# Optimization experiments

Hardware: AMD Instinct MI355X
Metric: run time of the kernel (lower is better)

The kernel has to match this reference:

```python
import jax, jax.numpy as jnp
import numpy as np
import math

H = 16          # num heads
D = 64          # size_per_head
HID = H * D     # 1024
ROT = 32        # rotary_hsize <= D//2


def setup_inputs() -> dict:
    key = jax.random.key(0)
    ks = jax.random.split(key, 10)
    B, S = 2, 2048
    x = jax.random.normal(ks[0], (B, S, HID), dtype=jnp.float32)
    sinusoids = jax.random.normal(ks[1], (B, 2, S, ROT), dtype=jnp.float32)
    attention_bias = jnp.zeros((B, 1, S, S), dtype=jnp.float32)
    scale = 1.0 / math.sqrt(HID)
    Wq = jax.random.normal(ks[2], (HID, HID), dtype=jnp.float32) * scale
    bq = jnp.zeros((HID,), dtype=jnp.float32)
    Wk = jax.random.normal(ks[3], (HID, HID), dtype=jnp.float32) * scale
    bk = jnp.zeros((HID,), dtype=jnp.float32)
    Wv = jax.random.normal(ks[4], (HID, HID), dtype=jnp.float32) * scale
    bv = jnp.zeros((HID,), dtype=jnp.float32)
    Wo = jax.random.normal(ks[5], (HID, HID), dtype=jnp.float32) * scale
    return {"x": x, "sinusoids": sinusoids, "attention_bias": attention_bias,
            "Wq": Wq, "bq": bq, "Wk": Wk, "bk": bk, "Wv": Wv, "bv": bv, "Wo": Wo}


def _apply_rotary(qk, sin, cos):
    # qk: [B,S,H,D]; sin/cos: [B,S,1,ROT]
    r = qk[..., :ROT]
    # stack([-even, odd], -1).reshape -> interleaved (-x0, x1, -x2, x3, ...)
    rt = jnp.stack([-r[..., ::2], r[..., 1::2]], axis=-1).reshape(r.shape)
    return jnp.concatenate([r * cos + rt * sin, qk[..., ROT:]], axis=-1)


def reference(x, sinusoids, attention_bias, Wq, bq, Wk, bk, Wv, bv, Wo):
    B, S, _ = x.shape
    q = (x @ Wq + bq).reshape(B, S, H, D)
    k = (x @ Wk + bk).reshape(B, S, H, D)
    v = (x @ Wv + bv).reshape(B, S, H, D)
    sin = sinusoids[..., 0, :, None, :]  # [B,S,1,ROT]
    cos = sinusoids[..., 1, :, None, :]
    q = _apply_rotary(q, sin, cos)
    k = _apply_rotary(k, sin, cos)
    q = q / math.sqrt(D)
    scores = jnp.einsum('bqhd,bkhd->bhqk', q, k) + attention_bias
    probs = jax.nn.softmax(scores, axis=-1)
    out = jnp.einsum('bhqk,bkhd->bqhd', probs, v).reshape(B, S, HID)
    return out @ Wo
```

## Files before the change

### kernel.cpp

```cpp
#include <hip/hip_runtime.h>
#include <hip/hip_bf16.h>

#define H_   16
#define D_   64
#define HID  1024
#define S_   2048
#define B_   2
#define M_   (B_*S_)
#define ROT  32
#define LOG2E 1.44269504088896341f
#define QSCALE (0.125f * LOG2E)

typedef __bf16 bf16x8 __attribute__((ext_vector_type(8)));
typedef float  f32x4  __attribute__((ext_vector_type(4)));

#define XB_OFF   0u
#define WQT_OFF  (8u<<20)
#define WKT_OFF  (10u<<20)
#define WVT_OFF  (12u<<20)
#define WOT_OFF  (14u<<20)
#define F_OFF    (16u<<20)
#define QH_OFF   ((16u<<20) + (1u<<19))
#define KH_OFF   (QH_OFF + (8u<<20))
#define VT_OFF   (KH_OFF + (8u<<20))
#define AB_OFF   (VT_OFF + (8u<<20))

__device__ __forceinline__ float fexp2(float x) {
#if __has_builtin(__builtin_amdgcn_exp2f)
  return __builtin_amdgcn_exp2f(x);
#else
  return __expf(x * 0.69314718055994531f);
#endif
}

__device__ __forceinline__ unsigned pk2(float a, float b) {
  union { unsigned u; __bf16 h[2]; } w;
  w.h[0] = (__bf16)a; w.h[1] = (__bf16)b;
  return w.u;
}

__global__ __launch_bounds__(256) void prep_kernel(const float* __restrict__ x,
                                                   const float* __restrict__ sinu,
                                                   const float* __restrict__ abias,
                                                   const float* __restrict__ W0, const float* __restrict__ W1,
                                                   const float* __restrict__ W2, const float* __restrict__ W3,
                                                   __hip_bfloat16* __restrict__ xb,
                                                   float* __restrict__ F,
                                                   __hip_bfloat16* __restrict__ T0, __hip_bfloat16* __restrict__ T1,
                                                   __hip_bfloat16* __restrict__ T2, __hip_bfloat16* __restrict__ T3,
                                                   int* __restrict__ flag) {
  __shared__ float tile[32][33];
  int idx = blockIdx.x;
  int tid = threadIdx.x;
  if (idx < 4096) {
    int i = (idx * 256 + tid) * 4;
    float4 v = *(const float4*)(x + i);
    union { __hip_bfloat16 h[4]; uint2 u; } o;
    o.h[0] = __float2bfloat16(v.x);
    o.h[1] = __float2bfloat16(v.y);
    o.h[2] = __float2bfloat16(v.z);
    o.h[3] = __float2bfloat16(v.w);
    *(uint2*)(xb + i) = o.u;
  } else if (idx < 4608) {
    int i = (idx - 4096) * 256 + tid;
    int d  = i & (ROT-1);
    int bs = i >> 5;
    int s  = bs & (S_-1);
    int b  = bs >> 11;
    float sn = sinu[(((size_t)b*2 + 0)*S_ + s)*ROT + d];
    float cs = sinu[(((size_t)b*2 + 1)*S_ + s)*ROT + d];
    F[i] = cs + ((d & 1) ? sn : -sn);
  } else if (idx < 8704) {
    int widx = idx - 4608;
    int z    = widx >> 10;
    int rem  = widx & 1023;
    const float* W = (z==0) ? W0 : (z==1) ? W1 : (z==2) ? W2 : W3;
    __hip_bfloat16* T = (z==0) ? T0 : (z==1) ? T1 : (z==2) ? T2 : T3;
    int bx = (rem & 31) * 32;
    int by = (rem >> 5) * 32;
    int tx = tid & 31, ty = tid >> 5;
    #pragma unroll
    for (int i = 0; i < 4; i++)
      tile[ty + i*8][tx] = W[(size_t)(by + ty + i*8)*HID + bx + tx];
    __syncthreads();
    #pragma unroll
    for (int i = 0; i < 4; i++)
      T[(size_t)(bx + ty + i*8)*HID + by + tx] = __float2bfloat16(tile[tx][ty + i*8]);
  } else {
    size_t i = ((size_t)(idx - 8704) * 256 + tid) * 16;
    const uint4* p = (const uint4*)(abias + i);
    unsigned acc = 0;
    #pragma unroll
    for (int j = 0; j < 4; j++) {
      uint4 u = p[j];
      acc |= u.x | u.y | u.z | u.w;
    }
    if (acc) *flag = 1;
  }
}

__global__ __launch_bounds__(256) void qkv_kernel(const __hip_bfloat16* __restrict__ A,
                                                  const __hip_bfloat16* __restrict__ Bt,
                                                  const float* __restrict__ bq,
                                                  const float* __restrict__ bk,
                                                  const float* __restrict__ bv,
                                                  const float* __restrict__ F,
                                                  __hip_bfloat16* __restrict__ Qh,
                                                  __hip_bfloat16* __restrict__ Kh,
                                                  __hip_bfloat16* __restrict__ Vt) {
  __shared__ __align__(16) __bf16 Asm[2][128*32];
  __shared__ __align__(16) __bf16 Bsm[2][128*32];
  int tid  = threadIdx.x;
  int lane = tid & 63;
  int wv   = tid >> 6;
  int lr   = lane & 15;
  int qd   = lane >> 4;
  int row0 = blockIdx.y * 128;
  int col0 = blockIdx.x * 128;
  int wrow = (wv >> 1) * 64;
  int wcol = (wv & 1) * 64;

  int cg = ((tid & 3) ^ ((tid >> 2) & 3)) * 8;
  const __bf16* Ag = (const __bf16*)A  + (size_t)(row0 + (tid >> 2)) * HID + cg;
  const __bf16* Bg = (const __bf16*)Bt + (size_t)(col0 + (tid >> 2)) * HID + cg;

  f32x4 acc[4][4] = {};

  auto stage = [&](int buf, int k0) {
    __builtin_amdgcn_global_load_lds(Ag + k0,                  &Asm[buf][wv*512],        16, 0, 0);
    __builtin_amdgcn_global_load_lds(Ag + (size_t)64*HID + k0, &Asm[buf][2048 + wv*512], 16, 0, 0);
    __builtin_amdgcn_global_load_lds(Bg + k0,                  &Bsm[buf][wv*512],        16, 0, 0);
    __builtin_amdgcn_global_load_lds(Bg + (size_t)64*HID + k0, &Bsm[buf][2048 + wv*512], 16, 0, 0);
  };

  stage(0, 0);
  int buf = 0;
  for (int k0 = 0; k0 < HID; k0 += 32, buf ^= 1) {
    __syncthreads();
    if (k0 + 32 < HID) stage(buf ^ 1, k0 + 32);
    const __bf16* As = &Asm[buf][0];
    const __bf16* Bs = &Bsm[buf][0];
    bf16x8 a[4], b[4];
    #pragma unroll
    for (int i = 0; i < 4; i++) {
      int row = wrow + i*16 + lr;
      a[i] = *(const bf16x8*)(As + row*32 + ((qd ^ (row & 3)) * 8));
    }
    #pragma unroll
    for (int t = 0; t < 4; t++) {
      int row = wcol + t*16 + lr;
      b[t] = *(const bf16x8*)(Bs + row*32 + ((qd ^ (row & 3)) * 8));
    }
    #pragma unroll
    for (int i = 0; i < 4; i++)
      #pragma unroll
      for (int t = 0; t < 4; t++)
        acc[i][t] = __builtin_amdgcn_mfma_f32_16x16x32_bf16(a[i], b[t], acc[i][t], 0, 0, 0);
  }

  int proj = col0 >> 10;
  int nb   = (col0 & 1023) + wcol;
  const float* bias = (proj == 0) ? bq : ((proj == 1) ? bk : bv);
  #pragma unroll
  for (int i = 0; i < 4; i++) {
    #pragma unroll
    for (int t = 0; t < 4; t++) {
      int nl = nb + t*16 + lr;
      int h  = nl >> 6, d = nl & 63;
      if (proj == 2) {
        int m0 = row0 + wrow + i*16 + qd*4;
        int b2 = m0 >> 11, s0 = m0 & (S_-1);
        union { uint2 u; __bf16 hh[4]; } w;
        #pragma unroll
        for (int r = 0; r < 4; r++)
          w.hh[r] = (__bf16)(acc[i][t][r] + bias[nl]);
        int pos = (s0 & ~31) | ((s0 & 12) << 1) | ((s0 >> 2) & 4);
        *(uint2*)((__bf16*)Vt + ((size_t)(b2*H_ + h)*D_ + d)*S_ + pos) = w.u;
      } else {
        __hip_bfloat16* dst = (proj == 0) ? Qh : Kh;
        #pragma unroll
        for (int r = 0; r < 4; r++) {
          int m = row0 + wrow + i*16 + qd*4 + r;
          int b2 = m >> 11, s = m & (S_-1);
          float v = acc[i][t][r] + bias[nl];
          if (d < ROT) v *= F[(size_t)(b2*S_ + s)*ROT + d];
          if (proj == 0) v *= QSCALE;
          dst[((size_t)(b2*H_ + h)*S_ + s)*D_ + d] = __float2bfloat16(v);
        }
      }
    }
  }
}

__global__ __launch_bounds__(256) void gemm_o64(const __hip_bfloat16* __restrict__ A,
                                                const __hip_bfloat16* __restrict__ Bt,
                                                float* __restrict__ outf) {
  __shared__ __align__(16) __bf16 Asm[2][128*32];
  __shared__ __align__(16) __bf16 Bsm[2][64*32];
  int tid  = threadIdx.x;
  int lane = tid & 63;
  int wv   = tid >> 6;
  int lr   = lane & 15;
  int qd   = lane >> 4;
  int row0 = blockIdx.y * 128;
  int col0 = blockIdx.x * 64;
  int cg = ((tid & 3) ^ ((tid >> 2) & 3)) * 8;
  const __bf16* Ag = (const __bf16*)A  + (size_t)(row0 + (tid >> 2)) * HID + cg;
  const __bf16* Bg = (const __bf16*)Bt + (size_t)(col0 + (tid >> 2)) * HID + cg;

  f32x4 acc[2][4] = {};
  auto stage = [&](int buf, int k0) {
    __builtin_amdgcn_global_load_lds(Ag + k0,                  &Asm[buf][wv*512],        16, 0, 0);
    __builtin_amdgcn_global_load_lds(Ag + (size_t)64*HID + k0, &Asm[buf][2048 + wv*512], 16, 0, 0);
    __builtin_amdgcn_global_load_lds(Bg + k0,                  &Bsm[buf][wv*512],        16, 0, 0);
  };
  stage(0, 0);
  int buf = 0;
  for (int k0 = 0; k0 < HID; k0 += 32, buf ^= 1) {
    __syncthreads();
    if (k0 + 32 < HID) stage(buf ^ 1, k0 + 32);
    const __bf16* As = &Asm[buf][0];
    const __bf16* Bs = &Bsm[buf][0];
    bf16x8 a[2], b[4];
    #pragma unroll
    for (int i = 0; i < 2; i++) {
      int row = wv*32 + i*16 + lr;
      a[i] = *(const bf16x8*)(As + row*32 + ((qd ^ (row & 3)) * 8));
    }
    #pragma unroll
    for (int t = 0; t < 4; t++) {
      int row = t*16 + lr;
      b[t] = *(const bf16x8*)(Bs + row*32 + ((qd ^ (row & 3)) * 8));
    }
    #pragma unroll
    for (int i = 0; i < 2; i++)
      #pragma unroll
      for (int t = 0; t < 4; t++)
        acc[i][t] = __builtin_amdgcn_mfma_f32_16x16x32_bf16(a[i], b[t], acc[i][t], 0, 0, 0);
  }
  #pragma unroll
  for (int i = 0; i < 2; i++)
    #pragma unroll
    for (int t = 0; t < 4; t++)
      #pragma unroll
      for (int r = 0; r < 4; r++) {
        int m = row0 + wv*32 + i*16 + qd*4 + r;
        int n = col0 + t*16 + lr;
        outf[(size_t)m*HID + n] = acc[i][t][r];
      }
}

__global__ __launch_bounds__(256) void flash_kernel(const __hip_bfloat16* __restrict__ Qh,
                                                    const __hip_bfloat16* __restrict__ Kh,
                                                    const __hip_bfloat16* __restrict__ Vt,
                                                    const float* __restrict__ abias,
                                                    const int* __restrict__ flag,
                                                    __hip_bfloat16* __restrict__ Ab) {
  __shared__ __align__(16) __bf16 Ksm[2][64*64];
  __shared__ __align__(16) __bf16 Vsm[2][64*64];
  int tid  = threadIdx.x;
  int lane = tid & 63;
  int wv   = tid >> 6;
  int lr   = lane & 15;
  int qd   = lane >> 4;
  int idx  = blockIdx.x;
  int xcd  = idx & 7;
  int slot = idx >> 3;
  int bh   = xcd * 4 + (slot >> 4);
  int qblk = slot & 15;
  int b  = bh >> 4;
  int h  = bh & 15;
  int q0 = qblk * 128 + wv * 32;

  const __bf16* Kbase = (const __bf16*)Kh + (size_t)bh*S_*D_;
  const __bf16* Vbase = (const __bf16*)Vt + (size_t)bh*D_*S_;

  const __bf16* Qp = (const __bf16*)Qh + ((size_t)bh*S_ + q0 + lr)*D_ + qd*8;
  bf16x8 qa00 = *(const bf16x8*)(Qp);
  bf16x8 qa01 = *(const bf16x8*)(Qp + 32);
  bf16x8 qa10 = *(const bf16x8*)(Qp + 16*D_);
  bf16x8 qa11 = *(const bf16x8*)(Qp + 16*D_ + 32);

  int hasbias = *flag;
  const float* bp0 = abias + (size_t)b*S_*S_ + (size_t)(q0 + lr)*S_;
  const float* bp1 = bp0 + (size_t)16*S_;

  int rowb = tid >> 3;
  int cg8  = ((tid & 7) ^ (rowb & 7)) * 8;

  auto stageKV = [&](int bf, int kt2) {
    __builtin_amdgcn_global_load_lds(Kbase + (size_t)(kt2 + rowb)*D_ + cg8,      &Ksm[bf][wv*512],        16, 0, 0);
    __builtin_amdgcn_global_load_lds(Kbase + (size_t)(kt2 + 32 + rowb)*D_ + cg8, &Ksm[bf][2048 + wv*512], 16, 0, 0);
    __builtin_amdgcn_global_load_lds(Vbase + (size_t)rowb*S_ + kt2 + cg8,        &Vsm[bf][wv*512],        16, 0, 0);
    __builtin_amdgcn_global_load_lds(Vbase + (size_t)(32 + rowb)*S_ + kt2 + cg8, &Vsm[bf][2048 + wv*512], 16, 0, 0);
  };

  f32x4 oacc0[4] = {}, oacc1[4] = {};
  float lsum0 = 0.f, lsum1 = 0.f;
  int sw = lr & 7;

  union Pu { bf16x8 v; unsigned u[4]; };
  Pu pb00 = {}, pb01 = {}, pb10 = {}, pb11 = {};
  bf16x8 vp0[4], vp1[4];

  stageKV(0, 0);
  int buf = 0;
  for (int kt = 0; kt < S_; kt += 64, buf ^= 1) {
    __syncthreads();
    if (kt + 64 < S_) stageKV(buf ^ 1, kt + 64);

    bf16x8 kf0[4], kf1[4];
    #pragma unroll
    for (int c = 0; c < 4; c++) {
      const __bf16* Kr = &Ksm[buf][(c*16 + lr)*64];
      kf0[c] = *(const bf16x8*)(Kr + ((qd       ^ sw) * 8));
      kf1[c] = *(const bf16x8*)(Kr + (((4 + qd) ^ sw) * 8));
    }

    if (kt > 0) {
      __builtin_amdgcn_s_setprio(1);
      #pragma unroll
      for (int t = 0; t < 4; t++) {
        oacc0[t] = __builtin_amdgcn_mfma_f32_16x16x32_bf16(vp0[t], pb00.v, oacc0[t], 0, 0, 0);
        oacc0[t] = __builtin_amdgcn_mfma_f32_16x16x32_bf16(vp1[t], pb01.v, oacc0[t], 0, 0, 0);
        oacc1[t] = __builtin_amdgcn_mfma_f32_16x16x32_bf16(vp0[t], pb10.v, oacc1[t], 0, 0, 0);
        oacc1[t] = __builtin_amdgcn_mfma_f32_16x16x32_bf16(vp1[t], pb11.v, oacc1[t], 0, 0, 0);
      }
      __builtin_amdgcn_s_setprio(0);
    }

    f32x4 s0[4], s1[4];
    __builtin_amdgcn_s_setprio(1);
    #pragma unroll
    for (int c = 0; c < 4; c++) {
      f32x4 z = {};
      z     = __builtin_amdgcn_mfma_f32_16x16x32_bf16(kf0[c], qa00, z, 0, 0, 0);
      s0[c] = __builtin_amdgcn_mfma_f32_16x16x32_bf16(kf1[c], qa01, z, 0, 0, 0);
      f32x4 z2 = {};
      z2    = __builtin_amdgcn_mfma_f32_16x16x32_bf16(kf0[c], qa10, z2, 0, 0, 0);
      s1[c] = __builtin_amdgcn_mfma_f32_16x16x32_bf16(kf1[c], qa11, z2, 0, 0, 0);
    }
    __builtin_amdgcn_s_setprio(0);

    if (hasbias) {
      #pragma unroll
      for (int c = 0; c < 4; c++) {
        float4 b0 = *(const float4*)(bp0 + kt + c*16 + qd*4);
        float4 b1 = *(const float4*)(bp1 + kt + c*16 + qd*4);
        s0[c][0] += b0.x*LOG2E; s0[c][1] += b0.y*LOG2E; s0[c][2] += b0.z*LOG2E; s0[c][3] += b0.w*LOG2E;
        s1[c][0] += b1.x*LOG2E; s1[c][1] += b1.y*LOG2E; s1[c][2] += b1.z*LOG2E; s1[c][3] += b1.w*LOG2E;
      }
    }

    #pragma unroll
    for (int c = 0; c < 2; c++) {
      float p0 = fexp2(s0[c][0]), p1 = fexp2(s0[c][1]), p2 = fexp2(s0[c][2]), p3 = fexp2(s0[c][3]);
      lsum0 += (p0 + p1) + (p2 + p3);
      pb00.u[2*c]   = pk2(p0, p1);
      pb00.u[2*c+1] = pk2(p2, p3);
      float r0 = fexp2(s1[c][0]), r1 = fexp2(s1[c][1]), r2 = fexp2(s1[c][2]), r3 = fexp2(s1[c][3]);
      lsum1 += (r0 + r1) + (r2 + r3);
      pb10.u[2*c]   = pk2(r0, r1);
      pb10.u[2*c+1] = pk2(r2, r3);
    }
    #pragma unroll
    for (int c = 2; c < 4; c++) {
      float p0 = fexp2(s0[c][0]), p1 = fexp2(s0[c][1]), p2 = fexp2(s0[c][2]), p3 = fexp2(s0[c][3]);
      lsum0 += (p0 + p1) + (p2 + p3);
      pb01.u[2*(c-2)]   = pk2(p0, p1);
      pb01.u[2*(c-2)+1] = pk2(p2, p3);
      float r0 = fexp2(s1[c][0]), r1 = fexp2(s1[c][1]), r2 = fexp2(s1[c][2]), r3 = fexp2(s1[c][3]);
      lsum1 += (r0 + r1) + (r2 + r3);
      pb11.u[2*(c-2)]   = pk2(r0, r1);
      pb11.u[2*(c-2)+1] = pk2(r2, r3);
    }

    #pragma unroll
    for (int t = 0; t < 4; t++) {
      const __bf16* Vr = &Vsm[buf][(t*16 + lr)*64];
      vp0[t] = *(const bf16x8*)(Vr + ((qd       ^ sw) * 8));
      vp1[t] = *(const bf16x8*)(Vr + (((4 + qd) ^ sw) * 8));
    }
  }

  __builtin_amdgcn_s_setprio(1);
  #pragma unroll
  for (int t = 0; t < 4; t++) {
    oacc0[t] = __builtin_amdgcn_mfma_f32_16x16x32_bf16(vp0[t], pb00.v, oacc0[t], 0, 0, 0);
    oacc0[t] = __builtin_amdgcn_mfma_f32_16x16x32_bf16(vp1[t], pb01.v, oacc0[t], 0, 0, 0);
    oacc1[t] = __builtin_amdgcn_mfma_f32_16x16x32_bf16(vp0[t], pb10.v, oacc1[t], 0, 0, 0);
    oacc1[t] = __builtin_amdgcn_mfma_f32_16x16x32_bf16(vp1[t], pb11.v, oacc1[t], 0, 0, 0);
  }
  __builtin_amdgcn_s_setprio(0);

  lsum0 += __shfl_xor(lsum0, 16); lsum0 += __shfl_xor(lsum0, 32);
  lsum1 += __shfl_xor(lsum1, 16); lsum1 += __shfl_xor(lsum1, 32);
  float inv0 = 1.0f / lsum0;
  float inv1 = 1.0f / lsum1;
  size_t ro0 = ((size_t)(b*S_ + q0 + lr))*HID + h*D_;
  size_t ro1 = ((size_t)(b*S_ + q0 + 16 + lr))*HID + h*D_;
  #pragma unroll
  for (int t = 0; t < 4; t++) {
    union { uint2 u; __bf16 hh[4]; } w0, w1;
    #pragma unroll
    for (int r = 0; r < 4; r++) {
      w0.hh[r] = (__bf16)(oacc0[t][r]*inv0);
      w1.hh[r] = (__bf16)(oacc1[t][r]*inv1);
    }
    *(uint2*)((__bf16*)Ab + ro0 + t*16 + qd*4) = w0.u;
    *(uint2*)((__bf16*)Ab + ro1 + t*16 + qd*4) = w1.u;
  }
}

extern "C" void kernel_launch(void* const* d_in, const int* in_sizes, int n_in,
                              void* d_out, int out_size, void* d_ws, size_t ws_size,
                              hipStream_t stream) {
  (void)in_sizes; (void)n_in; (void)out_size; (void)ws_size;
  const float* x     = (const float*)d_in[0];
  const float* sinu  = (const float*)d_in[1];
  const float* abias = (const float*)d_in[2];
  const float* Wq    = (const float*)d_in[3];
  const float* bq    = (const float*)d_in[4];
  const float* Wk    = (const float*)d_in[5];
  const float* bk    = (const float*)d_in[6];
  const float* Wv    = (const float*)d_in[7];
  const float* bv    = (const float*)d_in[8];
  const float* Wo    = (const float*)d_in[9];

  char* ws = (char*)d_ws;
  __hip_bfloat16* Xb  = (__hip_bfloat16*)(ws + XB_OFF);
  __hip_bfloat16* Wqt = (__hip_bfloat16*)(ws + WQT_OFF);
  __hip_bfloat16* Wkt = (__hip_bfloat16*)(ws + WKT_OFF);
  __hip_bfloat16* Wvt = (__hip_bfloat16*)(ws + WVT_OFF);
  __hip_bfloat16* Wot = (__hip_bfloat16*)(ws + WOT_OFF);
  float*          F   = (float*)(ws + F_OFF);
  __hip_bfloat16* Qh  = (__hip_bfloat16*)(ws + QH_OFF);
  __hip_bfloat16* Kh  = (__hip_bfloat16*)(ws + KH_OFF);
  __hip_bfloat16* Vt  = (__hip_bfloat16*)(ws + VT_OFF);
  __hip_bfloat16* Ab  = (__hip_bfloat16*)(ws + AB_OFF);
  int* flag = (int*)d_out;

  hipMemsetAsync(flag, 0, 4, stream);
  prep_kernel<<<10752, 256, 0, stream>>>(x, sinu, abias, Wq, Wk, Wv, Wo,
                                         Xb, F, Wqt, Wkt, Wvt, Wot, flag);

  qkv_kernel<<<dim3(3*HID/128, M_/128), 256, 0, stream>>>(
      Xb, Wqt, bq, bk, bv, F, Qh, Kh, Vt);

  flash_kernel<<<dim3(512), 256, 0, stream>>>(Qh, Kh, Vt, abias, flag, Ab);

  gemm_o64<<<dim3(HID/64, M_/128), 256, 0, stream>>>(Ab, Wot, (float*)d_out);
}
```

Before: 220.1 us.

## Halve flash-attention query tile per wave and double grid for occupancy

Each wave in the attention kernel now handles 16 query rows instead of 32, so a block covers 64 queries and the grid doubles to 1024 blocks, with launch bounds requesting 4 blocks per CU. The aim is more parallelism and fewer registers per thread, giving better latency hiding with 512 blocks on a 256-CU part. In exchange, every K/V tile staged into LDS is reused by half as many queries, which doubles K/V global traffic and the LDS fragment reads per unit of MFMA work.

```diff
diff --git a/kernel.cpp b/kernel.cpp
--- a/kernel.cpp
+++ b/kernel.cpp
@@ -250,7 +250,7 @@
       }
 }
 
-__global__ __launch_bounds__(256) void flash_kernel(const __hip_bfloat16* __restrict__ Qh,
+__global__ __launch_bounds__(256, 4) void flash_kernel(const __hip_bfloat16* __restrict__ Qh,
                                                     const __hip_bfloat16* __restrict__ Kh,
                                                     const __hip_bfloat16* __restrict__ Vt,
                                                     const float* __restrict__ abias,
@@ -266,11 +266,11 @@
   int idx  = blockIdx.x;
   int xcd  = idx & 7;
   int slot = idx >> 3;
-  int bh   = xcd * 4 + (slot >> 4);
-  int qblk = slot & 15;
+  int bh   = xcd * 4 + (slot >> 5);
+  int qblk = slot & 31;
   int b  = bh >> 4;
   int h  = bh & 15;
-  int q0 = qblk * 128 + wv * 32;
+  int q0 = qblk * 64 + wv * 16;
 
   const __bf16* Kbase = (const __bf16*)Kh + (size_t)bh*S_*D_;
   const __bf16* Vbase = (const __bf16*)Vt + (size_t)bh*D_*S_;
@@ -278,12 +278,9 @@
   const __bf16* Qp = (const __bf16*)Qh + ((size_t)bh*S_ + q0 + lr)*D_ + qd*8;
   bf16x8 qa00 = *(const bf16x8*)(Qp);
   bf16x8 qa01 = *(const bf16x8*)(Qp + 32);
-  bf16x8 qa10 = *(const bf16x8*)(Qp + 16*D_);
-  bf16x8 qa11 = *(const bf16x8*)(Qp + 16*D_ + 32);
 
   int hasbias = *flag;
   const float* bp0 = abias + (size_t)b*S_*S_ + (size_t)(q0 + lr)*S_;
-  const float* bp1 = bp0 + (size_t)16*S_;
 
   int rowb = tid >> 3;
   int cg8  = ((tid & 7) ^ (rowb & 7)) * 8;
@@ -295,12 +292,12 @@
     __builtin_amdgcn_global_load_lds(Vbase + (size_t)(32 + rowb)*S_ + kt2 + cg8, &Vsm[bf][2048 + wv*512], 16, 0, 0);
   };
 
-  f32x4 oacc0[4] = {}, oacc1[4] = {};
-  float lsum0 = 0.f, lsum1 = 0.f;
+  f32x4 oacc0[4] = {};
+  float lsum0 = 0.f;
   int sw = lr & 7;
 
   union Pu { bf16x8 v; unsigned u[4]; };
-  Pu pb00 = {}, pb01 = {}, pb10 = {}, pb11 = {};
+  Pu pb00 = {}, pb01 = {};
   bf16x8 vp0[4], vp1[4];
 
   stageKV(0, 0);
@@ -323,22 +320,17 @@
       for (int t = 0; t < 4; t++) {
         oacc0[t] = __builtin_amdgcn_mfma_f32_16x16x32_bf16(vp0[t], pb00.v, oacc0[t], 0, 0, 0);
         oacc0[t] = __builtin_amdgcn_mfma_f32_16x16x32_bf16(vp1[t], pb01.v, oacc0[t], 0, 0, 0);
-        oacc1[t] = __builtin_amdgcn_mfma_f32_16x16x32_bf16(vp0[t], pb10.v, oacc1[t], 0, 0, 0);
-        oacc1[t] = __builtin_amdgcn_mfma_f32_16x16x32_bf16(vp1[t], pb11.v, oacc1[t], 0, 0, 0);
       }
       __builtin_amdgcn_s_setprio(0);
     }
 
-    f32x4 s0[4], s1[4];
+    f32x4 s0[4];
     __builtin_amdgcn_s_setprio(1);
     #pragma unroll
     for (int c = 0; c < 4; c++) {
       f32x4 z = {};
       z     = __builtin_amdgcn_mfma_f32_16x16x32_bf16(kf0[c], qa00, z, 0, 0, 0);
       s0[c] = __builtin_amdgcn_mfma_f32_16x16x32_bf16(kf1[c], qa01, z, 0, 0, 0);
-      f32x4 z2 = {};
-      z2    = __builtin_amdgcn_mfma_f32_16x16x32_bf16(kf0[c], qa10, z2, 0, 0, 0);
-      s1[c] = __builtin_amdgcn_mfma_f32_16x16x32_bf16(kf1[c], qa11, z2, 0, 0, 0);
     }
     __builtin_amdgcn_s_setprio(0);
 
@@ -346,9 +338,7 @@
       #pragma unroll
       for (int c = 0; c < 4; c++) {
         float4 b0 = *(const float4*)(bp0 + kt + c*16 + qd*4);
-        float4 b1 = *(const float4*)(bp1 + kt + c*16 + qd*4);
         s0[c][0] += b0.x*LOG2E; s0[c][1] += b0.y*LOG2E; s0[c][2] += b0.z*LOG2E; s0[c][3] += b0.w*LOG2E;
-        s1[c][0] += b1.x*LOG2E; s1[c][1] += b1.y*LOG2E; s1[c][2] += b1.z*LOG2E; s1[c][3] += b1.w*LOG2E;
       }
     }
 
@@ -358,10 +348,6 @@
       lsum0 += (p0 + p1) + (p2 + p3);
       pb00.u[2*c]   = pk2(p0, p1);
       pb00.u[2*c+1] = pk2(p2, p3);
-      float r0 = fexp2(s1[c][0]), r1 = fexp2(s1[c][1]), r2 = fexp2(s1[c][2]), r3 = fexp2(s1[c][3]);
-      lsum1 += (r0 + r1) + (r2 + r3);
-      pb10.u[2*c]   = pk2(r0, r1);
-      pb10.u[2*c+1] = pk2(r2, r3);
     }
     #pragma unroll
     for (int c = 2; c < 4; c++) {
@@ -369,10 +355,6 @@
       lsum0 += (p0 + p1) + (p2 + p3);
       pb01.u[2*(c-2)]   = pk2(p0, p1);
       pb01.u[2*(c-2)+1] = pk2(p2, p3);
-      float r0 = fexp2(s1[c][0]), r1 = fexp2(s1[c][1]), r2 = fexp2(s1[c][2]), r3 = fexp2(s1[c][3]);
-      lsum1 += (r0 + r1) + (r2 + r3);
-      pb11.u[2*(c-2)]   = pk2(r0, r1);
-      pb11.u[2*(c-2)+1] = pk2(r2, r3);
     }
 
     #pragma unroll
@@ -388,27 +370,19 @@
   for (int t = 0; t < 4; t++) {
     oacc0[t] = __builtin_amdgcn_mfma_f32_16x16x32_bf16(vp0[t], pb00.v, oacc0[t], 0, 0, 0);
     oacc0[t] = __builtin_amdgcn_mfma_f32_16x16x32_bf16(vp1[t], pb01.v, oacc0[t], 0, 0, 0);
-    oacc1[t] = __builtin_amdgcn_mfma_f32_16x16x32_bf16(vp0[t], pb10.v, oacc1[t], 0, 0, 0);
-    oacc1[t] = __builtin_amdgcn_mfma_f32_16x16x32_bf16(vp1[t], pb11.v, oacc1[t], 0, 0, 0);
   }
   __builtin_amdgcn_s_setprio(0);
 
   lsum0 += __shfl_xor(lsum0, 16); lsum0 += __shfl_xor(lsum0, 32);
-  lsum1 += __shfl_xor(lsum1, 16); lsum1 += __shfl_xor(lsum1, 32);
   float inv0 = 1.0f / lsum0;
-  float inv1 = 1.0f / lsum1;
   size_t ro0 = ((size_t)(b*S_ + q0 + lr))*HID + h*D_;
-  size_t ro1 = ((size_t)(b*S_ + q0 + 16 + lr))*HID + h*D_;
   #pragma unroll
   for (int t = 0; t < 4; t++) {
-    union { uint2 u; __bf16 hh[4]; } w0, w1;
-    #pragma unroll
-    for (int r = 0; r < 4; r++) {
+    union { uint2 u; __bf16 hh[4]; } w0;
+    #pragma unroll
+    for (int r = 0; r < 4; r++)
       w0.hh[r] = (__bf16)(oacc0[t][r]*inv0);
-      w1.hh[r] = (__bf16)(oacc1[t][r]*inv1);
-    }
     *(uint2*)((__bf16*)Ab + ro0 + t*16 + qd*4) = w0.u;
-    *(uint2*)((__bf16*)Ab + ro1 + t*16 + qd*4) = w1.u;
   }
 }
 
@@ -447,7 +421,7 @@
   qkv_kernel<<<dim3(3*HID/128, M_/128), 256, 0, stream>>>(
       Xb, Wqt, bq, bk, bv, F, Qh, Kh, Vt);
 
-  flash_kernel<<<dim3(512), 256, 0, stream>>>(Qh, Kh, Vt, abias, flag, Ab);
+  flash_kernel<<<dim3(1024), 256, 0, stream>>>(Qh, Kh, Vt, abias, flag, Ab);
 
   gemm_o64<<<dim3(HID/64, M_/128), 256, 0, stream>>>(Ab, Wot, (float*)d_out);
 }
```

New measurement: 226.6 us. 1.03x slower.

## Split flash attention KV range across two wave groups per block and merge

Applied to the files above, without the earlier changes.

Doubles the flash kernel block to 512 threads. Each half of the block processes half of the key/value sequence for the same 128 query rows, using its own double-buffered LDS. At the end, the second half writes its partial output accumulators and row sums into LDS, and the first half merges them and normalizes. This raises wave count per block to improve latency hiding and CU utilisation on a 512-block grid. The cost is double the LDS, an extra merge through LDS, and two more barriers. The merge skips max rescaling because the softmax here uses no running max.

```diff
diff --git a/kernel.cpp b/kernel.cpp
--- a/kernel.cpp
+++ b/kernel.cpp
@@ -250,17 +250,19 @@
       }
 }
 
-__global__ __launch_bounds__(256) void flash_kernel(const __hip_bfloat16* __restrict__ Qh,
+__global__ __launch_bounds__(512, 4) void flash_kernel(const __hip_bfloat16* __restrict__ Qh,
                                                     const __hip_bfloat16* __restrict__ Kh,
                                                     const __hip_bfloat16* __restrict__ Vt,
                                                     const float* __restrict__ abias,
                                                     const int* __restrict__ flag,
                                                     __hip_bfloat16* __restrict__ Ab) {
-  __shared__ __align__(16) __bf16 Ksm[2][64*64];
-  __shared__ __align__(16) __bf16 Vsm[2][64*64];
+  __shared__ __align__(16) __bf16 Ksm[2][2][64*64];
+  __shared__ __align__(16) __bf16 Vsm[2][2][64*64];
   int tid  = threadIdx.x;
   int lane = tid & 63;
   int wv   = tid >> 6;
+  int wvh  = wv & 3;
+  int kh   = wv >> 2;
   int lr   = lane & 15;
   int qd   = lane >> 4;
   int idx  = blockIdx.x;
@@ -270,7 +272,8 @@
   int qblk = slot & 15;
   int b  = bh >> 4;
   int h  = bh & 15;
-  int q0 = qblk * 128 + wv * 32;
+  int q0 = qblk * 128 + wvh * 32;
+  int kt0 = kh * (S_/2);
 
   const __bf16* Kbase = (const __bf16*)Kh + (size_t)bh*S_*D_;
   const __bf16* Vbase = (const __bf16*)Vt + (size_t)bh*D_*S_;
@@ -285,14 +288,15 @@
   const float* bp0 = abias + (size_t)b*S_*S_ + (size_t)(q0 + lr)*S_;
   const float* bp1 = bp0 + (size_t)16*S_;
 
-  int rowb = tid >> 3;
-  int cg8  = ((tid & 7) ^ (rowb & 7)) * 8;
+  int tidh = tid & 255;
+  int rowb = tidh >> 3;
+  int cg8  = ((tidh & 7) ^ (rowb & 7)) * 8;
 
   auto stageKV = [&](int bf, int kt2) {
-    __builtin_amdgcn_global_load_lds(Kbase + (size_t)(kt2 + rowb)*D_ + cg8,      &Ksm[bf][wv*512],        16, 0, 0);
-    __builtin_amdgcn_global_load_lds(Kbase + (size_t)(kt2 + 32 + rowb)*D_ + cg8, &Ksm[bf][2048 + wv*512], 16, 0, 0);
-    __builtin_amdgcn_global_load_lds(Vbase + (size_t)rowb*S_ + kt2 + cg8,        &Vsm[bf][wv*512],        16, 0, 0);
-    __builtin_amdgcn_global_load_lds(Vbase + (size_t)(32 + rowb)*S_ + kt2 + cg8, &Vsm[bf][2048 + wv*512], 16, 0, 0);
+    __builtin_amdgcn_global_load_lds(Kbase + (size_t)(kt2 + rowb)*D_ + cg8,      &Ksm[kh][bf][wvh*512],        16, 0, 0);
+    __builtin_amdgcn_global_load_lds(Kbase + (size_t)(kt2 + 32 + rowb)*D_ + cg8, &Ksm[kh][bf][2048 + wvh*512], 16, 0, 0);
+    __builtin_amdgcn_global_load_lds(Vbase + (size_t)rowb*S_ + kt2 + cg8,        &Vsm[kh][bf][wvh*512],        16, 0, 0);
+    __builtin_amdgcn_global_load_lds(Vbase + (size_t)(32 + rowb)*S_ + kt2 + cg8, &Vsm[kh][bf][2048 + wvh*512], 16, 0, 0);
   };
 
   f32x4 oacc0[4] = {}, oacc1[4] = {};
@@ -303,21 +307,21 @@
   Pu pb00 = {}, pb01 = {}, pb10 = {}, pb11 = {};
   bf16x8 vp0[4], vp1[4];
 
-  stageKV(0, 0);
+  stageKV(0, kt0);
   int buf = 0;
-  for (int kt = 0; kt < S_; kt += 64, buf ^= 1) {
+  for (int kt = kt0; kt < kt0 + S_/2; kt += 64, buf ^= 1) {
     __syncthreads();
-    if (kt + 64 < S_) stageKV(buf ^ 1, kt + 64);
+    if (kt + 64 < kt0 + S_/2) stageKV(buf ^ 1, kt + 64);
 
     bf16x8 kf0[4], kf1[4];
     #pragma unroll
     for (int c = 0; c < 4; c++) {
-      const __bf16* Kr = &Ksm[buf][(c*16 + lr)*64];
+      const __bf16* Kr = &Ksm[kh][buf][(c*16 + lr)*64];
       kf0[c] = *(const bf16x8*)(Kr + ((qd       ^ sw) * 8));
       kf1[c] = *(const bf16x8*)(Kr + (((4 + qd) ^ sw) * 8));
     }
 
-    if (kt > 0) {
+    if (kt > kt0) {
       __builtin_amdgcn_s_setprio(1);
       #pragma unroll
       for (int t = 0; t < 4; t++) {
@@ -377,7 +381,7 @@
 
     #pragma unroll
     for (int t = 0; t < 4; t++) {
-      const __bf16* Vr = &Vsm[buf][(t*16 + lr)*64];
+      const __bf16* Vr = &Vsm[kh][buf][(t*16 + lr)*64];
       vp0[t] = *(const bf16x8*)(Vr + ((qd       ^ sw) * 8));
       vp1[t] = *(const bf16x8*)(Vr + (((4 + qd) ^ sw) * 8));
     }
@@ -393,22 +397,41 @@
   }
   __builtin_amdgcn_s_setprio(0);
 
+  __syncthreads();
   lsum0 += __shfl_xor(lsum0, 16); lsum0 += __shfl_xor(lsum0, 32);
   lsum1 += __shfl_xor(lsum1, 16); lsum1 += __shfl_xor(lsum1, 32);
-  float inv0 = 1.0f / lsum0;
-  float inv1 = 1.0f / lsum1;
-  size_t ro0 = ((size_t)(b*S_ + q0 + lr))*HID + h*D_;
-  size_t ro1 = ((size_t)(b*S_ + q0 + 16 + lr))*HID + h*D_;
-  #pragma unroll
-  for (int t = 0; t < 4; t++) {
-    union { uint2 u; __bf16 hh[4]; } w0, w1;
-    #pragma unroll
-    for (int r = 0; r < 4; r++) {
-      w0.hh[r] = (__bf16)(oacc0[t][r]*inv0);
-      w1.hh[r] = (__bf16)(oacc1[t][r]*inv1);
-    }
-    *(uint2*)((__bf16*)Ab + ro0 + t*16 + qd*4) = w0.u;
-    *(uint2*)((__bf16*)Ab + ro1 + t*16 + qd*4) = w1.u;
+  float* mrg = (float*)&Ksm[0][0][0];
+  float* ml  = (float*)&Vsm[0][0][0];
+  int mb = (wvh*64 + lane)*32;
+  int mx = lane & 31;
+  if (kh == 1) {
+    #pragma unroll
+    for (int t = 0; t < 4; t++)
+      #pragma unroll
+      for (int r = 0; r < 4; r++) {
+        mrg[mb + ((t*4 + r) ^ mx)]      = oacc0[t][r];
+        mrg[mb + ((16 + t*4 + r) ^ mx)] = oacc1[t][r];
+      }
+    ml[wvh*128 + lane]      = lsum0;
+    ml[wvh*128 + 64 + lane] = lsum1;
+  }
+  __syncthreads();
+  if (kh == 0) {
+    float inv0 = 1.0f / (lsum0 + ml[wvh*128 + lane]);
+    float inv1 = 1.0f / (lsum1 + ml[wvh*128 + 64 + lane]);
+    size_t ro0 = ((size_t)(b*S_ + q0 + lr))*HID + h*D_;
+    size_t ro1 = ((size_t)(b*S_ + q0 + 16 + lr))*HID + h*D_;
+    #pragma unroll
+    for (int t = 0; t < 4; t++) {
+      union { uint2 u; __bf16 hh[4]; } w0, w1;
+      #pragma unroll
+      for (int r = 0; r < 4; r++) {
+        w0.hh[r] = (__bf16)((oacc0[t][r] + mrg[mb + ((t*4 + r) ^ mx)]) * inv0);
+        w1.hh[r] = (__bf16)((oacc1[t][r] + mrg[mb + ((16 + t*4 + r) ^ mx)]) * inv1);
+      }
+      *(uint2*)((__bf16*)Ab + ro0 + t*16 + qd*4) = w0.u;
+      *(uint2*)((__bf16*)Ab + ro1 + t*16 + qd*4) = w1.u;
+    }
   }
 }
 
@@ -447,7 +470,7 @@
   qkv_kernel<<<dim3(3*HID/128, M_/128), 256, 0, stream>>>(
       Xb, Wqt, bq, bk, bv, F, Qh, Kh, Vt);
 
-  flash_kernel<<<dim3(512), 256, 0, stream>>>(Qh, Kh, Vt, abias, flag, Ab);
+  flash_kernel<<<dim3(512), 512, 0, stream>>>(Qh, Kh, Vt, abias, flag, Ab);
 
   gemm_o64<<<dim3(HID/64, M_/128), 256, 0, stream>>>(Ab, Wot, (float*)d_out);
 }
```

Result: slower. 290.1 us (+31.8%).
